# Kernel optimization log

Measured on AMD Instinct MI355X. Metric: run time of the kernel, lower is better.

Reference implementation:

```python
import jax, jax.numpy as jnp
import numpy as np

B, L, RNN, ATT = 128, 1024, 1024, 512

def setup_inputs() -> dict:
    key = jax.random.key(0)
    ks = jax.random.split(key, 6)
    h = jax.random.normal(ks[0], (B, RNN), dtype=jnp.float32)
    att_feats1 = jax.random.normal(ks[1], (B, L, RNN), dtype=jnp.float32)
    att_feats2 = jax.random.normal(ks[2], (B, L, ATT), dtype=jnp.float32)
    att_masks = jax.random.randint(ks[3], (B, L), 0, 2).astype(jnp.float32)
    att_masks = att_masks.at[:, 0].set(1.0)  # avoid all-zero rows (div by zero)
    W_h2att = jax.random.normal(ks[4], (ATT, RNN), dtype=jnp.float32) * (1.0 / np.sqrt(RNN))
    b_h2att = jnp.zeros((ATT,), dtype=jnp.float32)
    w_alpha = jax.random.normal(ks[5], (ATT,), dtype=jnp.float32) * (1.0 / np.sqrt(ATT))
    b_alpha = jnp.zeros((), dtype=jnp.float32)
    return {"h": h, "att_feats1": att_feats1, "att_feats2": att_feats2,
            "att_masks": att_masks, "W_h2att": W_h2att, "b_h2att": b_h2att,
            "w_alpha": w_alpha, "b_alpha": b_alpha}

def reference(h, att_feats1, att_feats2, att_masks, W_h2att, b_h2att, w_alpha, b_alpha):
    # h2att: [B, RNN] -> [B, ATT]
    att_h = h @ W_h2att.T + b_h2att
    # broadcast add over L, tanh, score via alpha_net: [B, L]
    dot = jnp.einsum('bla,a->bl', jnp.tanh(att_feats2 + att_h[:, None, :]), w_alpha) + b_alpha
    weight = jax.nn.softmax(dot, axis=1)
    # masked renormalization
    weight = weight * att_masks
    weight = weight / jnp.sum(weight, axis=1, keepdims=True)
    # weighted sum of att_feats1: [B, RNN]
    att = jnp.einsum('bl,bld->bd', weight, att_feats1)
    return att
```

## Files before the change

kernel.cpp:

```cpp
#include <hip/hip_runtime.h>

#define B_   128
#define L_   1024
#define RNN_ 1024
#define ATT_ 512

__device__ __forceinline__ float fast_tanh(float x) {
    float e = __expf(2.0f * x);
    return 1.0f - __fdividef(2.0f, e + 1.0f);
}

__global__ __launch_bounds__(256) void k1_h2att(
        const float* __restrict__ h, const float* __restrict__ W,
        const float* __restrict__ bias, float* __restrict__ att_h) {
    __shared__ float hs[16][64];
    __shared__ float ws[64][65];
    const int a0 = blockIdx.x * 64;
    const int b0 = blockIdx.y * 16;
    const int t  = threadIdx.x;
    const int a_local = t & 63;
    const int brow    = (t >> 6) * 4;

    float acc[4] = {0.f, 0.f, 0.f, 0.f};

    for (int k0 = 0; k0 < RNN_; k0 += 64) {
        {
            int r = t >> 4, c = (t & 15) * 4;
            const float4 v = *(const float4*)&h[(size_t)(b0 + r) * RNN_ + k0 + c];
            hs[r][c + 0] = v.x; hs[r][c + 1] = v.y;
            hs[r][c + 2] = v.z; hs[r][c + 3] = v.w;
        }
        #pragma unroll
        for (int j = 0; j < 4; j++) {
            int r = (t >> 4) + 16 * j, c = (t & 15) * 4;
            const float4 v = *(const float4*)&W[(size_t)(a0 + r) * RNN_ + k0 + c];
            ws[r][c + 0] = v.x; ws[r][c + 1] = v.y;
            ws[r][c + 2] = v.z; ws[r][c + 3] = v.w;
        }
        __syncthreads();
        #pragma unroll 8
        for (int kk = 0; kk < 64; kk++) {
            const float wv = ws[a_local][kk];
            #pragma unroll
            for (int j = 0; j < 4; j++)
                acc[j] = fmaf(hs[brow + j][kk], wv, acc[j]);
        }
        __syncthreads();
    }
    const float bs = bias[a0 + a_local];
    #pragma unroll
    for (int j = 0; j < 4; j++)
        att_h[(size_t)(b0 + brow + j) * ATT_ + a0 + a_local] = acc[j] + bs;
}

__global__ __launch_bounds__(256) void k2_score(
        const float* __restrict__ f2, const float* __restrict__ att_h,
        const float* __restrict__ w_alpha, const float* __restrict__ b_alpha,
        float* __restrict__ dot) {
    const int wid  = (blockIdx.x * 256 + threadIdx.x) >> 6;
    const int lane = threadIdx.x & 63;
    const int b = wid >> 10;
    const int l = wid & (L_ - 1);

    const float4* f  = (const float4*)f2 + (size_t)(b * L_ + l) * (ATT_ / 4);
    const float4* ah = (const float4*)att_h + (size_t)b * (ATT_ / 4);
    const float4* wa = (const float4*)w_alpha;

    float s = 0.f;
    #pragma unroll
    for (int i = 0; i < 2; i++) {
        const int idx = lane + i * 64;
        const float4 x = f[idx];
        const float4 a = ah[idx];
        const float4 w = wa[idx];
        s = fmaf(fast_tanh(x.x + a.x), w.x, s);
        s = fmaf(fast_tanh(x.y + a.y), w.y, s);
        s = fmaf(fast_tanh(x.z + a.z), w.z, s);
        s = fmaf(fast_tanh(x.w + a.w), w.w, s);
    }
    #pragma unroll
    for (int off = 32; off > 0; off >>= 1)
        s += __shfl_xor(s, off, 64);
    if (lane == 0)
        dot[b * L_ + l] = s + b_alpha[0];
}

__global__ __launch_bounds__(256) void k3_softmax(
        const float* __restrict__ dot, const float* __restrict__ mask,
        float* __restrict__ weight) {
    const int b = blockIdx.x, t = threadIdx.x;
    const int base = b * L_;
    const int wv = t >> 6, lane = t & 63;
    __shared__ float sred[4];

    float v[4];
    float mx = -3.4e38f;
    #pragma unroll
    for (int j = 0; j < 4; j++) {
        v[j] = dot[base + t + 256 * j];
        mx = fmaxf(mx, v[j]);
    }
    #pragma unroll
    for (int off = 32; off > 0; off >>= 1)
        mx = fmaxf(mx, __shfl_xor(mx, off, 64));
    if (lane == 0) sred[wv] = mx;
    __syncthreads();
    mx = fmaxf(fmaxf(sred[0], sred[1]), fmaxf(sred[2], sred[3]));
    __syncthreads();

    float e[4], s = 0.f;
    #pragma unroll
    for (int j = 0; j < 4; j++) {
        e[j] = __expf(v[j] - mx) * mask[base + t + 256 * j];
        s += e[j];
    }
    #pragma unroll
    for (int off = 32; off > 0; off >>= 1)
        s += __shfl_xor(s, off, 64);
    if (lane == 0) sred[wv] = s;
    __syncthreads();
    s = sred[0] + sred[1] + sred[2] + sred[3];

    const float inv = 1.0f / s;
    #pragma unroll
    for (int j = 0; j < 4; j++)
        weight[base + t + 256 * j] = e[j] * inv;
}

__global__ __launch_bounds__(256) void k4_wsum(
        const float* __restrict__ f1, const float* __restrict__ weight,
        float* __restrict__ out) {
    const int b = blockIdx.x, lc = blockIdx.y, t = threadIdx.x;
    const float* wrow = weight + b * L_ + lc * 64;
    const float4* base =
        (const float4*)f1 + ((size_t)b * L_ + lc * 64) * (RNN_ / 4) + t;

    float4 acc = make_float4(0.f, 0.f, 0.f, 0.f);
    #pragma unroll 8
    for (int l = 0; l < 64; l++) {
        const float w = wrow[l];
        const float4 x = base[(size_t)l * (RNN_ / 4)];
        acc.x = fmaf(w, x.x, acc.x);
        acc.y = fmaf(w, x.y, acc.y);
        acc.z = fmaf(w, x.z, acc.z);
        acc.w = fmaf(w, x.w, acc.w);
    }
    float* o = out + b * RNN_ + t * 4;
    atomicAdd(o + 0, acc.x);
    atomicAdd(o + 1, acc.y);
    atomicAdd(o + 2, acc.z);
    atomicAdd(o + 3, acc.w);
}

extern "C" void kernel_launch(void* const* d_in, const int* in_sizes, int n_in,
                              void* d_out, int out_size, void* d_ws, size_t ws_size,
                              hipStream_t stream) {
    const float* h       = (const float*)d_in[0];
    const float* f1      = (const float*)d_in[1];
    const float* f2      = (const float*)d_in[2];
    const float* mask    = (const float*)d_in[3];
    const float* W       = (const float*)d_in[4];
    const float* b_h2att = (const float*)d_in[5];
    const float* w_alpha = (const float*)d_in[6];
    const float* b_alpha = (const float*)d_in[7];

    float* att_h  = (float*)d_ws;
    float* dot    = att_h + (size_t)B_ * ATT_;
    float* weight = dot + (size_t)B_ * L_;
    float* out    = (float*)d_out;

    k1_h2att<<<dim3(ATT_ / 64, B_ / 16), 256, 0, stream>>>(h, W, b_h2att, att_h);

    k2_score<<<(B_ * L_) / 4, 256, 0, stream>>>(f2, att_h, w_alpha, b_alpha, dot);

    k3_softmax<<<B_, 256, 0, stream>>>(dot, mask, weight);

    hipMemsetAsync(out, 0, (size_t)out_size * sizeof(float), stream);
    k4_wsum<<<dim3(B_, 16), 256, 0, stream>>>(f1, weight, out);
}
```

Baseline: 872.9 us.

## Fold softmax normalization into weighted-sum kernel and process two rows per wave in scoring

The scoring kernel now has each wave compute two sequence positions, reusing the att_h and w_alpha loads and halving the grid. The softmax kernel now writes only a per-batch max and inverse sum. The weighted-sum kernel recomputes the normalized weights into shared memory from dot, mask and those stats, so the weight array is no longer written and read back. The weighted-sum chunk per block grows from 64 to 128 positions, which halves the atomic adds but also halves the number of blocks and so reduces parallelism.

New measurement: 870.7 us. About the same (-0.3%).

```diff
diff --git a/kernel.cpp b/kernel.cpp
--- a/kernel.cpp
+++ b/kernel.cpp
@@ -59,35 +59,45 @@
         float* __restrict__ dot) {
     const int wid  = (blockIdx.x * 256 + threadIdx.x) >> 6;
     const int lane = threadIdx.x & 63;
-    const int b = wid >> 10;
-    const int l = wid & (L_ - 1);
+    const int b  = wid >> 9;
+    const int l0 = (wid & 511) << 1;
 
-    const float4* f  = (const float4*)f2 + (size_t)(b * L_ + l) * (ATT_ / 4);
+    const float4* f  = (const float4*)f2 + (size_t)(b * L_ + l0) * (ATT_ / 4);
     const float4* ah = (const float4*)att_h + (size_t)b * (ATT_ / 4);
     const float4* wa = (const float4*)w_alpha;
 
-    float s = 0.f;
+    float s0 = 0.f, s1 = 0.f;
     #pragma unroll
     for (int i = 0; i < 2; i++) {
         const int idx = lane + i * 64;
-        const float4 x = f[idx];
         const float4 a = ah[idx];
         const float4 w = wa[idx];
-        s = fmaf(fast_tanh(x.x + a.x), w.x, s);
-        s = fmaf(fast_tanh(x.y + a.y), w.y, s);
-        s = fmaf(fast_tanh(x.z + a.z), w.z, s);
-        s = fmaf(fast_tanh(x.w + a.w), w.w, s);
+        const float4 x = f[idx];
+        const float4 y = f[idx + ATT_ / 4];
+        s0 = fmaf(fast_tanh(x.x + a.x), w.x, s0);
+        s0 = fmaf(fast_tanh(x.y + a.y), w.y, s0);
+        s0 = fmaf(fast_tanh(x.z + a.z), w.z, s0);
+        s0 = fmaf(fast_tanh(x.w + a.w), w.w, s0);
+        s1 = fmaf(fast_tanh(y.x + a.x), w.x, s1);
+        s1 = fmaf(fast_tanh(y.y + a.y), w.y, s1);
+        s1 = fmaf(fast_tanh(y.z + a.z), w.z, s1);
+        s1 = fmaf(fast_tanh(y.w + a.w), w.w, s1);
     }
     #pragma unroll
-    for (int off = 32; off > 0; off >>= 1)
-        s += __shfl_xor(s, off, 64);
-    if (lane == 0)
-        dot[b * L_ + l] = s + b_alpha[0];
+    for (int off = 32; off > 0; off >>= 1) {
+        s0 += __shfl_xor(s0, off, 64);
+        s1 += __shfl_xor(s1, off, 64);
+    }
+    if (lane == 0) {
+        const float ba = b_alpha[0];
+        dot[b * L_ + l0 + 0] = s0 + ba;
+        dot[b * L_ + l0 + 1] = s1 + ba;
+    }
 }
 
-__global__ __launch_bounds__(256) void k3_softmax(
+__global__ __launch_bounds__(256) void k3_stats(
         const float* __restrict__ dot, const float* __restrict__ mask,
-        float* __restrict__ weight) {
+        float2* __restrict__ stats) {
     const int b = blockIdx.x, t = threadIdx.x;
     const int base = b * L_;
     const int wv = t >> 6, lane = t & 63;
@@ -108,42 +118,45 @@
     mx = fmaxf(fmaxf(sred[0], sred[1]), fmaxf(sred[2], sred[3]));
     __syncthreads();
 
-    float e[4], s = 0.f;
+    float s = 0.f;
     #pragma unroll
-    for (int j = 0; j < 4; j++) {
-        e[j] = __expf(v[j] - mx) * mask[base + t + 256 * j];
-        s += e[j];
-    }
+    for (int j = 0; j < 4; j++)
+        s += __expf(v[j] - mx) * mask[base + t + 256 * j];
     #pragma unroll
     for (int off = 32; off > 0; off >>= 1)
         s += __shfl_xor(s, off, 64);
     if (lane == 0) sred[wv] = s;
     __syncthreads();
-    s = sred[0] + sred[1] + sred[2] + sred[3];
-
-    const float inv = 1.0f / s;
-    #pragma unroll
-    for (int j = 0; j < 4; j++)
-        weight[base + t + 256 * j] = e[j] * inv;
+    if (t == 0) {
+        const float stot = sred[0] + sred[1] + sred[2] + sred[3];
+        stats[b] = make_float2(mx, 1.0f / stot);
+    }
 }
 
 __global__ __launch_bounds__(256) void k4_wsum(
-        const float* __restrict__ f1, const float* __restrict__ weight,
+        const float* __restrict__ f1, const float* __restrict__ dot,
+        const float* __restrict__ mask, const float2* __restrict__ stats,
         float* __restrict__ out) {
     const int b = blockIdx.x, lc = blockIdx.y, t = threadIdx.x;
-    const float* wrow = weight + b * L_ + lc * 64;
+    __shared__ float w[128];
+    const float2 st = stats[b];
+    const int lbase = b * L_ + lc * 128;
+    if (t < 128)
+        w[t] = __expf(dot[lbase + t] - st.x) * mask[lbase + t] * st.y;
+    __syncthreads();
+
     const float4* base =
-        (const float4*)f1 + ((size_t)b * L_ + lc * 64) * (RNN_ / 4) + t;
+        (const float4*)f1 + ((size_t)b * L_ + lc * 128) * (RNN_ / 4) + t;
 
     float4 acc = make_float4(0.f, 0.f, 0.f, 0.f);
     #pragma unroll 8
-    for (int l = 0; l < 64; l++) {
-        const float w = wrow[l];
+    for (int l = 0; l < 128; l++) {
+        const float wv = w[l];
         const float4 x = base[(size_t)l * (RNN_ / 4)];
-        acc.x = fmaf(w, x.x, acc.x);
-        acc.y = fmaf(w, x.y, acc.y);
-        acc.z = fmaf(w, x.z, acc.z);
-        acc.w = fmaf(w, x.w, acc.w);
+        acc.x = fmaf(wv, x.x, acc.x);
+        acc.y = fmaf(wv, x.y, acc.y);
+        acc.z = fmaf(wv, x.z, acc.z);
+        acc.w = fmaf(wv, x.w, acc.w);
     }
     float* o = out + b * RNN_ + t * 4;
     atomicAdd(o + 0, acc.x);
@@ -164,17 +177,14 @@
     const float* w_alpha = (const float*)d_in[6];
     const float* b_alpha = (const float*)d_in[7];
 
-    float* att_h  = (float*)d_ws;
-    float* dot    = att_h + (size_t)B_ * ATT_;
-    float* weight = dot + (size_t)B_ * L_;
-    float* out    = (float*)d_out;
+    float*  att_h = (float*)d_ws;
+    float*  dot   = att_h + (size_t)B_ * ATT_;
+    float2* stats = (float2*)(dot + (size_t)B_ * L_);
+    float*  out   = (float*)d_out;
 
     k1_h2att<<<dim3(ATT_ / 64, B_ / 16), 256, 0, stream>>>(h, W, b_h2att, att_h);
-
-    k2_score<<<(B_ * L_) / 4, 256, 0, stream>>>(f2, att_h, w_alpha, b_alpha, dot);
-
-    k3_softmax<<<B_, 256, 0, stream>>>(dot, mask, weight);
-
+    k2_score<<<(B_ * L_ / 2) / 4, 256, 0, stream>>>(f2, att_h, w_alpha, b_alpha, dot);
+    k3_stats<<<B_, 256, 0, stream>>>(dot, mask, stats);
     hipMemsetAsync(out, 0, (size_t)out_size * sizeof(float), stream);
-    k4_wsum<<<dim3(B_, 16), 256, 0, stream>>>(f1, weight, out);
+    k4_wsum<<<dim3(B_, 8), 256, 0, stream>>>(f1, dot, mask, stats, out);
 }
```
